# Optimization experiments

Measured on AMD Instinct MI355X. Metric: run time of the kernel, lower is better.

The kernel has to match this reference:

```python
import jax, jax.numpy as jnp
import numpy as np
import math

B, S, D = 4, 2048, 1024

def setup_inputs() -> dict:
    key = jax.random.key(0)
    k_x, k_q, k_k, k_v = jax.random.split(key, 4)
    scale = 1.0 / math.sqrt(D)
    return {
        "x": jax.random.normal(k_x, (B, S, D), dtype=jnp.float32),
        "W_Q": jax.random.normal(k_q, (D, D), dtype=jnp.float32) * scale,
        "W_K": jax.random.normal(k_k, (D, D), dtype=jnp.float32) * scale,
        "W_V": jax.random.normal(k_v, (D, D), dtype=jnp.float32) * scale,
    }

def reference(x, W_Q, W_K, W_V):
    # nn.Linear(bias=False): y = x @ W.T
    Q = jnp.einsum('bsd,ed->bse', x, W_Q)
    K = jnp.einsum('bsd,ed->bse', x, W_K)
    V = jnp.einsum('bsd,ed->bse', x, W_V)
    scores = jnp.einsum('bqd,bkd->bqk', Q, K) / jnp.sqrt(jnp.asarray(Q.shape[-1], Q.dtype))
    weight = jax.nn.softmax(scores, axis=-1)  # [B,S,S]
    return jnp.einsum('bqk,bkd->bqd', weight, V)
```

## Files before the change

### kernel.cpp

```cpp
#include <hip/hip_runtime.h>
#include <stdint.h>

typedef __bf16 bf16;
typedef __bf16 bf16x8 __attribute__((ext_vector_type(8)));
typedef __bf16 bf16x4 __attribute__((ext_vector_type(4)));
typedef float f32x4 __attribute__((ext_vector_type(4)));

__device__ inline void gload_lds16(const void* g, void* l) {
  __builtin_amdgcn_global_load_lds(
      (__attribute__((address_space(1))) void*)g,
      (__attribute__((address_space(3))) void*)l, 16, 0, 0);
}

__global__ __launch_bounds__(256) void cvt_all(
    const float* __restrict__ x, const float* __restrict__ wq,
    const float* __restrict__ wk, const float* __restrict__ wv,
    bf16* __restrict__ xb, bf16* __restrict__ Wb) {
  const int NX = 2097152;
  const int NW = 262144;
  int i = blockIdx.x * 256 + threadIdx.x;
  const int stride = gridDim.x * 256;
  for (int p = i; p < NX + 3 * NW; p += stride) {
    const float* src; bf16* dst; int off;
    if (p < NX) { src = x; dst = xb; off = p; }
    else {
      int q = p - NX; int w = q >> 18; off = q & (NW - 1);
      src = (w == 0) ? wq : ((w == 1) ? wk : wv);
      dst = Wb + (long)w * 1048576;
    }
    float4 v = ((const float4*)src)[off];
    bf16x4 o;
    o[0] = (bf16)v.x; o[1] = (bf16)v.y; o[2] = (bf16)v.z; o[3] = (bf16)v.w;
    ((bf16x4*)dst)[off] = o;
  }
}

__global__ __launch_bounds__(512, 2) void projT(
    const bf16* __restrict__ Wg, const bf16* __restrict__ Xg,
    bf16* __restrict__ QKbuf, bf16* __restrict__ Vt)
{
  constexpr int BUFSZ = 40960;
  __shared__ alignas(16) char lds[2 * BUFSZ];
  const int tid = threadIdx.x;
  const int l = tid & 63;
  const int wv = tid >> 6;
  const int wm = wv >> 2;
  const int wn = wv & 3;
  const int fr = l & 15;
  const int kch = l >> 4;
  const int m0 = blockIdx.y * 384;
  const int n0 = blockIdx.x * 256;

  const int a_rd = fr * 128 + (((wm * 4 + kch) ^ (fr & 7)) << 4);
  const int b_rd = 24576 + (wn & 1) * 8192 + fr * 128 + ((((wn >> 1) * 4 + kch) ^ (fr & 7)) << 4);

  const int se = (tid & 7) ^ ((tid >> 3) & 7);
  const int s_rowA = (se >> 2) * 192 + (tid >> 3);
  const int s_rowB = (se >> 2) * 128 + (tid >> 3);
  const int s_k = (se & 3) * 8;
  const int wb16 = (tid & 448) * 16;

  const int NT = 32;
  f32x4 acc[12][4] = {};

  auto stageA = [&](int tile, int buf, int rd) {
    gload_lds16(Wg + (long)(m0 + s_rowA + rd * 64) * 1024 + tile * 32 + s_k,
                lds + buf * BUFSZ + rd * 8192 + wb16);
  };
  auto stageB = [&](int tile, int buf, int rd) {
    gload_lds16(Xg + (long)(n0 + s_rowB + rd * 64) * 1024 + tile * 32 + s_k,
                lds + buf * BUFSZ + 24576 + rd * 8192 + wb16);
  };

  stageA(0, 0, 0); stageB(0, 0, 0); stageA(0, 0, 1); stageB(0, 0, 1); stageA(0, 0, 2);
  stageA(1, 1, 0); stageB(1, 1, 0); stageA(1, 1, 1);
  asm volatile("s_waitcnt vmcnt(3)" ::: "memory");
  __builtin_amdgcn_sched_barrier(0);
  __builtin_amdgcn_s_barrier();

  for (int t = 0; t < NT; ++t) {
    const char* buf = lds + (t & 1) * BUFSZ;
    const int t1 = min(t + 1, NT - 1);
    const int t2 = min(t + 2, NT - 1);
    const int nb = (t & 1) ^ 1;
    const int cur = t & 1;

    bf16x8 bfg[4], af[4];
    stageA(t1, nb, 2); stageB(t1, nb, 1);
#pragma unroll
    for (int n = 0; n < 4; ++n) bfg[n] = *(const bf16x8*)(buf + n * 2048 + b_rd);
#pragma unroll
    for (int m = 0; m < 4; ++m) af[m] = *(const bf16x8*)(buf + m * 2048 + a_rd);
    __builtin_amdgcn_s_barrier();
    __builtin_amdgcn_s_setprio(1);
#pragma unroll
    for (int m = 0; m < 4; ++m)
#pragma unroll
      for (int n = 0; n < 4; ++n)
        acc[m][n] = __builtin_amdgcn_mfma_f32_16x16x32_bf16(af[m], bfg[n], acc[m][n], 0, 0, 0);
    __builtin_amdgcn_s_setprio(0);
    __builtin_amdgcn_s_barrier();
    stageA(t2, cur, 0); stageB(t2, cur, 0);
#pragma unroll
    for (int m = 0; m < 4; ++m) af[m] = *(const bf16x8*)(buf + 8192 + m * 2048 + a_rd);
    __builtin_amdgcn_s_barrier();
    __builtin_amdgcn_s_setprio(1);
#pragma unroll
    for (int m = 0; m < 4; ++m)
#pragma unroll
      for (int n = 0; n < 4; ++n)
        acc[4 + m][n] = __builtin_amdgcn_mfma_f32_16x16x32_bf16(af[m], bfg[n], acc[4 + m][n], 0, 0, 0);
    __builtin_amdgcn_s_setprio(0);
    __builtin_amdgcn_s_barrier();
    stageA(t2, cur, 1);
#pragma unroll
    for (int m = 0; m < 4; ++m) af[m] = *(const bf16x8*)(buf + 16384 + m * 2048 + a_rd);
    __builtin_amdgcn_s_barrier();
    __builtin_amdgcn_s_setprio(1);
#pragma unroll
    for (int m = 0; m < 4; ++m)
#pragma unroll
      for (int n = 0; n < 4; ++n)
        acc[8 + m][n] = __builtin_amdgcn_mfma_f32_16x16x32_bf16(af[m], bfg[n], acc[8 + m][n], 0, 0, 0);
    __builtin_amdgcn_s_setprio(0);
    asm volatile("s_waitcnt vmcnt(3)" ::: "memory");
    __builtin_amdgcn_sched_barrier(0);
    __builtin_amdgcn_s_barrier();
  }
  asm volatile("s_waitcnt vmcnt(0)" ::: "memory");

#pragma unroll
  for (int mf = 0; mf < 12; ++mf) {
    const int wrow = m0 + wm * 192 + (mf >> 2) * 64 + (mf & 3) * 16 + (l >> 4) * 4;
#pragma unroll
    for (int n = 0; n < 4; ++n) {
      const int xrow = n0 + wn * 64 + n * 16 + fr;
      if (wrow < 2048) {
        bf16x4 pk;
#pragma unroll
        for (int r = 0; r < 4; ++r) pk[r] = (bf16)acc[mf][n][r];
        *(bf16x4*)(QKbuf + (long)xrow * 2048 + wrow) = pk;
      } else {
        const int b = xrow >> 11;
        const int s = xrow & 2047;
#pragma unroll
        for (int r = 0; r < 4; ++r)
          Vt[(long)b * 2097152 + (long)(wrow - 2048 + r) * 2048 + s] = (bf16)acc[mf][n][r];
      }
    }
  }
}

__global__ __launch_bounds__(512, 2) void gemm8(
    const bf16* __restrict__ Ag, const bf16* __restrict__ Bg,
    bf16* __restrict__ Cg,
    long lda, long ldb, long ldc,
    long sA, long sB, long sC, int K, float scale)
{
  constexpr int BUFSZ = 65536;
  __shared__ alignas(16) char lds[2 * BUFSZ];
  const int tid = threadIdx.x;
  const int l = tid & 63;
  const int wv = tid >> 6;
  const int fr = l & 15;
  const int kch = l >> 4;
  const int m0 = blockIdx.y * 256;
  const int n0 = blockIdx.x * 256;
  const bf16* Ab = Ag + (long)blockIdx.z * sA;
  const bf16* Bb = Bg + (long)blockIdx.z * sB;

  const int wm = wv >> 2;
  const int wn = wv & 3;

  const int a_rd = fr * 128 + (((wm * 4 + kch) ^ (fr & 7)) << 4);
  const int b_rd = (wn & 1) * 8192 + fr * 128 + ((((wn >> 1) * 4 + kch) ^ (fr & 7)) << 4);

  const int se = (tid & 7) ^ ((tid >> 3) & 7);
  const int s_row = (se >> 2) * 128 + (tid >> 3);
  const int s_k = (se & 3) * 8;
  const int wb16 = (tid & 448) * 16;

  const int NT = K >> 6;
  f32x4 acc[8][4] = {};

  auto stageA = [&](int tile, int kh, int buf) {
#pragma unroll
    for (int rd = 0; rd < 2; ++rd)
      gload_lds16(Ab + (long)(m0 + s_row + rd * 64) * lda + tile * 64 + kh * 32 + s_k,
                  lds + buf * BUFSZ + kh * 16384 + rd * 8192 + wb16);
  };
  auto stageB = [&](int tile, int kh, int buf) {
#pragma unroll
    for (int rd = 0; rd < 2; ++rd)
      gload_lds16(Bb + (long)(n0 + s_row + rd * 64) * ldb + tile * 64 + kh * 32 + s_k,
                  lds + buf * BUFSZ + 32768 + kh * 16384 + rd * 8192 + wb16);
  };

  stageA(0, 0, 0); stageB(0, 0, 0); stageA(0, 1, 0); stageB(0, 1, 0);
  stageA(min(1, NT - 1), 0, 1); stageB(min(1, NT - 1), 0, 1);
  asm volatile("s_waitcnt vmcnt(4)" ::: "memory");
  __builtin_amdgcn_sched_barrier(0);
  __builtin_amdgcn_s_barrier();

  for (int t = 0; t < NT; ++t) {
    const char* bufA = lds + (t & 1) * BUFSZ;
    const char* bufB = bufA + 32768;
    const int t1 = min(t + 1, NT - 1);
    const int t2 = min(t + 2, NT - 1);
    const int nb = (t & 1) ^ 1;
    const int cur = t & 1;

    bf16x8 bfg[4], af[4];
    stageA(t1, 1, nb);
#pragma unroll
    for (int n = 0; n < 4; ++n) bfg[n] = *(const bf16x8*)(bufB + n * 2048 + b_rd);
#pragma unroll
    for (int m = 0; m < 4; ++m) af[m] = *(const bf16x8*)(bufA + m * 2048 + a_rd);
    __builtin_amdgcn_s_barrier();
    __builtin_amdgcn_s_setprio(1);
#pragma unroll
    for (int m = 0; m < 4; ++m)
#pragma unroll
      for (int n = 0; n < 4; ++n)
        acc[m][n] = __builtin_amdgcn_mfma_f32_16x16x32_bf16(af[m], bfg[n], acc[m][n], 0, 0, 0);
    __builtin_amdgcn_s_setprio(0);
    __builtin_amdgcn_s_barrier();
    stageB(t1, 1, nb);
#pragma unroll
    for (int m = 0; m < 4; ++m) af[m] = *(const bf16x8*)(bufA + 8192 + m * 2048 + a_rd);
    __builtin_amdgcn_s_barrier();
    __builtin_amdgcn_s_setprio(1);
#pragma unroll
    for (int m = 0; m < 4; ++m)
#pragma unroll
      for (int n = 0; n < 4; ++n)
        acc[4 + m][n] = __builtin_amdgcn_mfma_f32_16x16x32_bf16(af[m], bfg[n], acc[4 + m][n], 0, 0, 0);
    __builtin_amdgcn_s_setprio(0);
    __builtin_amdgcn_s_barrier();
    stageA(t2, 0, cur);
#pragma unroll
    for (int n = 0; n < 4; ++n) bfg[n] = *(const bf16x8*)(bufB + 16384 + n * 2048 + b_rd);
#pragma unroll
    for (int m = 0; m < 4; ++m) af[m] = *(const bf16x8*)(bufA + 16384 + m * 2048 + a_rd);
    __builtin_amdgcn_s_barrier();
    __builtin_amdgcn_s_setprio(1);
#pragma unroll
    for (int m = 0; m < 4; ++m)
#pragma unroll
      for (int n = 0; n < 4; ++n)
        acc[m][n] = __builtin_amdgcn_mfma_f32_16x16x32_bf16(af[m], bfg[n], acc[m][n], 0, 0, 0);
    __builtin_amdgcn_s_setprio(0);
    __builtin_amdgcn_s_barrier();
    stageB(t2, 0, cur);
#pragma unroll
    for (int m = 0; m < 4; ++m) af[m] = *(const bf16x8*)(bufA + 16384 + 8192 + m * 2048 + a_rd);
    __builtin_amdgcn_s_barrier();
    __builtin_amdgcn_s_setprio(1);
#pragma unroll
    for (int m = 0; m < 4; ++m)
#pragma unroll
      for (int n = 0; n < 4; ++n)
        acc[4 + m][n] = __builtin_amdgcn_mfma_f32_16x16x32_bf16(af[m], bfg[n], acc[4 + m][n], 0, 0, 0);
    __builtin_amdgcn_s_setprio(0);
    asm volatile("s_waitcnt vmcnt(4)" ::: "memory");
    __builtin_amdgcn_sched_barrier(0);
    __builtin_amdgcn_s_barrier();
  }
  asm volatile("s_waitcnt vmcnt(0)" ::: "memory");

#pragma unroll
  for (int mf = 0; mf < 8; ++mf) {
    const int row = m0 + wm * 128 + (mf >> 2) * 64 + (mf & 3) * 16 + (l >> 4) * 4;
#pragma unroll
    for (int n = 0; n < 4; ++n) {
      const int col = n0 + wn * 64 + n * 16 + fr;
      bf16* C = Cg + (long)blockIdx.z * sC;
#pragma unroll
      for (int r = 0; r < 4; ++r)
        C[(long)(row + r) * ldc + col] = (bf16)(acc[mf][n][r] * scale);
    }
  }
}

__global__ __launch_bounds__(256, 2) void gemm2h(
    const bf16* __restrict__ Ag, const bf16* __restrict__ Bg,
    float* __restrict__ Cg,
    long lda, long ldb, long ldc,
    long sA, long sB, long sC, int K)
{
  constexpr int BUFSZ = 32768;
  __shared__ alignas(16) char lds[2 * BUFSZ];
  const int tid = threadIdx.x;
  const int l = tid & 63;
  const int wv = tid >> 6;
  const int wm = wv >> 1, wn = wv & 1;
  const int fr = l & 15;
  const int kch = l >> 4;
  const int m0 = blockIdx.y * 128;
  const int n0 = blockIdx.x * 128;
  const bf16* Ab = Ag + (long)blockIdx.z * sA;
  const bf16* Bb = Bg + (long)blockIdx.z * sB;

  const int a_rd = fr * 128 + (((wm * 4 + kch) ^ (fr & 7)) << 4);
  const int b_rd = fr * 128 + (((wn * 4 + kch) ^ (fr & 7)) << 4);

  const int se = (tid & 7) ^ ((tid >> 3) & 7);
  const int s_row = (se >> 2) * 64 + (tid >> 3);
  const int s_k = (se & 3) * 8;
  const int wb16 = (tid >> 6) * 1024;

  const int NT = K >> 6;
  f32x4 acc[4][4] = {};

  auto stageA = [&](int tile, int kh, int buf) {
#pragma unroll
    for (int rd = 0; rd < 2; ++rd)
      gload_lds16(Ab + (long)(m0 + s_row + rd * 32) * lda + tile * 64 + kh * 32 + s_k,
                  lds + buf * BUFSZ + kh * 8192 + rd * 4096 + wb16);
  };
  auto stageB = [&](int tile, int kh, int buf) {
#pragma unroll
    for (int rd = 0; rd < 2; ++rd)
      gload_lds16(Bb + (long)(n0 + s_row + rd * 32) * ldb + tile * 64 + kh * 32 + s_k,
                  lds + buf * BUFSZ + 16384 + kh * 8192 + rd * 4096 + wb16);
  };

  stageA(0, 0, 0); stageB(0, 0, 0); stageA(0, 1, 0); stageB(0, 1, 0);
  stageA(min(1, NT - 1), 0, 1); stageB(min(1, NT - 1), 0, 1);
  asm volatile("s_waitcnt vmcnt(4)" ::: "memory");
  __builtin_amdgcn_sched_barrier(0);
  __builtin_amdgcn_s_barrier();

  for (int t = 0; t < NT; ++t) {
    const char* bufA = lds + (t & 1) * BUFSZ;
    const char* bufB = bufA + 16384;
    const int t1 = min(t + 1, NT - 1);
    const int t2 = min(t + 2, NT - 1);
    const int nb = (t & 1) ^ 1;
    const int cur = t & 1;

    bf16x8 bfg[4], af[4];
    stageA(t1, 1, nb); stageB(t1, 1, nb);
#pragma unroll
    for (int n = 0; n < 4; ++n) bfg[n] = *(const bf16x8*)(bufB + n * 2048 + b_rd);
#pragma unroll
    for (int m = 0; m < 4; ++m) af[m] = *(const bf16x8*)(bufA + m * 2048 + a_rd);
    __builtin_amdgcn_s_barrier();
    __builtin_amdgcn_s_setprio(1);
#pragma unroll
    for (int m = 0; m < 4; ++m)
#pragma unroll
      for (int n = 0; n < 4; ++n)
        acc[m][n] = __builtin_amdgcn_mfma_f32_16x16x32_bf16(af[m], bfg[n], acc[m][n], 0, 0, 0);
    __builtin_amdgcn_s_setprio(0);
    __builtin_amdgcn_s_barrier();
    stageA(t2, 0, cur); stageB(t2, 0, cur);
#pragma unroll
    for (int n = 0; n < 4; ++n) bfg[n] = *(const bf16x8*)(bufB + 8192 + n * 2048 + b_rd);
#pragma unroll
    for (int m = 0; m < 4; ++m) af[m] = *(const bf16x8*)(bufA + 8192 + m * 2048 + a_rd);
    __builtin_amdgcn_s_barrier();
    __builtin_amdgcn_s_setprio(1);
#pragma unroll
    for (int m = 0; m < 4; ++m)
#pragma unroll
      for (int n = 0; n < 4; ++n)
        acc[m][n] = __builtin_amdgcn_mfma_f32_16x16x32_bf16(af[m], bfg[n], acc[m][n], 0, 0, 0);
    __builtin_amdgcn_s_setprio(0);
    asm volatile("s_waitcnt vmcnt(4)" ::: "memory");
    __builtin_amdgcn_sched_barrier(0);
    __builtin_amdgcn_s_barrier();
  }
  asm volatile("s_waitcnt vmcnt(0)" ::: "memory");

#pragma unroll
  for (int mf = 0; mf < 4; ++mf) {
    const int row = m0 + wm * 64 + mf * 16 + (l >> 4) * 4;
#pragma unroll
    for (int n = 0; n < 4; ++n) {
      const int col = n0 + wn * 64 + n * 16 + fr;
      float* C = Cg + (long)blockIdx.z * sC;
#pragma unroll
      for (int r = 0; r < 4; ++r)
        C[(long)(row + r) * ldc + col] = acc[mf][n][r];
    }
  }
}

__global__ __launch_bounds__(256) void softmax_k(const bf16* __restrict__ Sm,
                                                 bf16* __restrict__ P, int cols) {
  __shared__ float red[8];
  const long row = blockIdx.x;
  const bf16* sr = Sm + row * (long)cols;
  bf16* pr = P + row * (long)cols;
  const int t = threadIdx.x;
  bf16x8 v = *(const bf16x8*)(sr + t * 8);
  float e[8];
#pragma unroll
  for (int j = 0; j < 8; ++j) e[j] = (float)v[j];
  float m = e[0];
#pragma unroll
  for (int j = 1; j < 8; ++j) m = fmaxf(m, e[j]);
#pragma unroll
  for (int o = 32; o; o >>= 1) m = fmaxf(m, __shfl_xor(m, o));
  if ((t & 63) == 0) red[t >> 6] = m;
  __syncthreads();
  m = fmaxf(fmaxf(red[0], red[1]), fmaxf(red[2], red[3]));
  float s = 0.f;
#pragma unroll
  for (int j = 0; j < 8; ++j) { e[j] = __expf(e[j] - m); s += e[j]; }
#pragma unroll
  for (int o = 32; o; o >>= 1) s += __shfl_xor(s, o);
  if ((t & 63) == 0) red[4 + (t >> 6)] = s;
  __syncthreads();
  s = red[4] + red[5] + red[6] + red[7];
  const float inv = 1.0f / s;
  bf16x8 o8;
#pragma unroll
  for (int j = 0; j < 8; ++j) o8[j] = (bf16)(e[j] * inv);
  *(bf16x8*)(pr + t * 8) = o8;
}

extern "C" void kernel_launch(void* const* d_in, const int* in_sizes, int n_in,
                              void* d_out, int out_size, void* d_ws, size_t ws_size,
                              hipStream_t stream) {
  const float* x  = (const float*)d_in[0];
  const float* Wq = (const float*)d_in[1];
  const float* Wk = (const float*)d_in[2];
  const float* Wv = (const float*)d_in[3];
  float* out = (float*)d_out;

  char* ws = (char*)d_ws;
  bf16* QKbuf = (bf16*)(ws);
  bf16* P     = (bf16*)(ws);
  bf16* Vt    = (bf16*)(ws + 33554432);
  bf16* scb   = (bf16*)(ws + 50331648);
  bf16* xb    = (bf16*)(ws + 50331648);
  bf16* Wb    = (bf16*)(ws + 67108864);

  dim3 b256(256, 1, 1), b512(512, 1, 1);

  cvt_all<<<2048, b256, 0, stream>>>(x, Wq, Wk, Wv, xb, Wb);

  projT<<<dim3(32, 8, 1), b512, 0, stream>>>(Wb, xb, QKbuf, Vt);

  gemm8<<<dim3(8, 8, 4), b512, 0, stream>>>(
      QKbuf, QKbuf + 1024, scb, 2048, 2048, 2048,
      4194304, 4194304, 4194304, 1024, 0.03125f);

  softmax_k<<<8192, b256, 0, stream>>>(scb, P, 2048);

  gemm2h<<<dim3(8, 16, 4), b256, 0, stream>>>(
      P, Vt, out, 2048, 2048, 1024,
      4194304, 2097152, 2097152, 2048);
}
```

Baseline: 167.6 us.

## Swap projection GEMM operand roles and drop redundant LDS barriers in GEMMs

The projection kernel is rewritten so that x is the M-side operand and the stacked weights are the N-side operand. Each wave now computes an 8x6 fragment tile over two sub-steps per K tile instead of 12x4 over three, and the QK outputs are written row-major with scalar stores while V^T gets packed vector stores. Separately, the barrier between the LDS fragment reads and the MFMA block is removed in the projection, gemm8 and gemm2h loops, which cuts per-iteration synchronisation. Removing those barriers relies on the remaining barriers and vmcnt waits to keep the double-buffered LDS reads safe, and there is a risk of a race if buffer reuse ordering was depending on them.

```diff
diff --git a/kernel.cpp b/kernel.cpp
--- a/kernel.cpp
+++ b/kernel.cpp
@@ -35,8 +35,8 @@
   }
 }
 
-__global__ __launch_bounds__(512, 2) void projT(
-    const bf16* __restrict__ Wg, const bf16* __restrict__ Xg,
+__global__ __launch_bounds__(512, 2) void projW(
+    const bf16* __restrict__ Xg, const bf16* __restrict__ Wg,
     bf16* __restrict__ QKbuf, bf16* __restrict__ Vt)
 {
   constexpr int BUFSZ = 40960;
@@ -48,104 +48,100 @@
   const int wn = wv & 3;
   const int fr = l & 15;
   const int kch = l >> 4;
-  const int m0 = blockIdx.y * 384;
-  const int n0 = blockIdx.x * 256;
+  const int m0 = blockIdx.y * 256;
+  const int n0 = blockIdx.x * 384;
 
   const int a_rd = fr * 128 + (((wm * 4 + kch) ^ (fr & 7)) << 4);
-  const int b_rd = 24576 + (wn & 1) * 8192 + fr * 128 + ((((wn >> 1) * 4 + kch) ^ (fr & 7)) << 4);
+  int b_off[6];
+#pragma unroll
+  for (int n = 0; n < 6; ++n) {
+    const int rowbase = wn * 96 + n * 16;
+    const int half = rowbase >= 192 ? 1 : 0;
+    b_off[n] = 16384 + (rowbase - half * 192 + fr) * 128 +
+               (((half * 4 + kch) ^ (fr & 7)) << 4);
+  }
 
   const int se = (tid & 7) ^ ((tid >> 3) & 7);
-  const int s_rowA = (se >> 2) * 192 + (tid >> 3);
-  const int s_rowB = (se >> 2) * 128 + (tid >> 3);
+  const int s_rowA = (se >> 2) * 128 + (tid >> 3);
+  const int s_rowB = (se >> 2) * 192 + (tid >> 3);
   const int s_k = (se & 3) * 8;
   const int wb16 = (tid & 448) * 16;
 
-  const int NT = 32;
-  f32x4 acc[12][4] = {};
+  f32x4 acc[8][6] = {};
 
   auto stageA = [&](int tile, int buf, int rd) {
-    gload_lds16(Wg + (long)(m0 + s_rowA + rd * 64) * 1024 + tile * 32 + s_k,
+    gload_lds16(Xg + (long)(m0 + s_rowA + rd * 64) * 1024 + tile * 32 + s_k,
                 lds + buf * BUFSZ + rd * 8192 + wb16);
   };
   auto stageB = [&](int tile, int buf, int rd) {
-    gload_lds16(Xg + (long)(n0 + s_rowB + rd * 64) * 1024 + tile * 32 + s_k,
-                lds + buf * BUFSZ + 24576 + rd * 8192 + wb16);
-  };
-
-  stageA(0, 0, 0); stageB(0, 0, 0); stageA(0, 0, 1); stageB(0, 0, 1); stageA(0, 0, 2);
-  stageA(1, 1, 0); stageB(1, 1, 0); stageA(1, 1, 1);
-  asm volatile("s_waitcnt vmcnt(3)" ::: "memory");
+    gload_lds16(Wg + (long)(n0 + s_rowB + rd * 64) * 1024 + tile * 32 + s_k,
+                lds + buf * BUFSZ + 16384 + rd * 8192 + wb16);
+  };
+
+  stageA(0, 0, 0); stageA(0, 0, 1);
+  stageB(0, 0, 0); stageB(0, 0, 1); stageB(0, 0, 2);
+  stageA(1, 1, 0);
+  stageB(1, 1, 0); stageB(1, 1, 1); stageB(1, 1, 2);
+  asm volatile("s_waitcnt vmcnt(4)" ::: "memory");
   __builtin_amdgcn_sched_barrier(0);
   __builtin_amdgcn_s_barrier();
 
-  for (int t = 0; t < NT; ++t) {
+  for (int t = 0; t < 32; ++t) {
     const char* buf = lds + (t & 1) * BUFSZ;
-    const int t1 = min(t + 1, NT - 1);
-    const int t2 = min(t + 2, NT - 1);
+    const int t1 = min(t + 1, 31);
+    const int t2 = min(t + 2, 31);
     const int nb = (t & 1) ^ 1;
     const int cur = t & 1;
 
-    bf16x8 bfg[4], af[4];
-    stageA(t1, nb, 2); stageB(t1, nb, 1);
-#pragma unroll
-    for (int n = 0; n < 4; ++n) bfg[n] = *(const bf16x8*)(buf + n * 2048 + b_rd);
+    bf16x8 bfg[6], af[4];
+    stageA(t1, nb, 1);
+    asm volatile("s_waitcnt vmcnt(5)" ::: "memory");
+    __builtin_amdgcn_sched_barrier(0);
+#pragma unroll
+    for (int n = 0; n < 6; ++n) bfg[n] = *(const bf16x8*)(buf + b_off[n]);
 #pragma unroll
     for (int m = 0; m < 4; ++m) af[m] = *(const bf16x8*)(buf + m * 2048 + a_rd);
-    __builtin_amdgcn_s_barrier();
-    __builtin_amdgcn_s_setprio(1);
-#pragma unroll
-    for (int m = 0; m < 4; ++m)
-#pragma unroll
-      for (int n = 0; n < 4; ++n)
+    __builtin_amdgcn_s_setprio(1);
+#pragma unroll
+    for (int m = 0; m < 4; ++m)
+#pragma unroll
+      for (int n = 0; n < 6; ++n)
         acc[m][n] = __builtin_amdgcn_mfma_f32_16x16x32_bf16(af[m], bfg[n], acc[m][n], 0, 0, 0);
     __builtin_amdgcn_s_setprio(0);
     __builtin_amdgcn_s_barrier();
-    stageA(t2, cur, 0); stageB(t2, cur, 0);
-#pragma unroll
-    for (int m = 0; m < 4; ++m) af[m] = *(const bf16x8*)(buf + 8192 + m * 2048 + a_rd);
-    __builtin_amdgcn_s_barrier();
-    __builtin_amdgcn_s_setprio(1);
-#pragma unroll
-    for (int m = 0; m < 4; ++m)
-#pragma unroll
-      for (int n = 0; n < 4; ++n)
+    stageA(t2, cur, 0);
+    stageB(t2, cur, 0); stageB(t2, cur, 1); stageB(t2, cur, 2);
+#pragma unroll
+    for (int m = 0; m < 4; ++m) af[m] = *(const bf16x8*)(buf + (4 + m) * 2048 + a_rd);
+    __builtin_amdgcn_s_setprio(1);
+#pragma unroll
+    for (int m = 0; m < 4; ++m)
+#pragma unroll
+      for (int n = 0; n < 6; ++n)
         acc[4 + m][n] = __builtin_amdgcn_mfma_f32_16x16x32_bf16(af[m], bfg[n], acc[4 + m][n], 0, 0, 0);
     __builtin_amdgcn_s_setprio(0);
     __builtin_amdgcn_s_barrier();
-    stageA(t2, cur, 1);
-#pragma unroll
-    for (int m = 0; m < 4; ++m) af[m] = *(const bf16x8*)(buf + 16384 + m * 2048 + a_rd);
-    __builtin_amdgcn_s_barrier();
-    __builtin_amdgcn_s_setprio(1);
-#pragma unroll
-    for (int m = 0; m < 4; ++m)
-#pragma unroll
-      for (int n = 0; n < 4; ++n)
-        acc[8 + m][n] = __builtin_amdgcn_mfma_f32_16x16x32_bf16(af[m], bfg[n], acc[8 + m][n], 0, 0, 0);
-    __builtin_amdgcn_s_setprio(0);
-    asm volatile("s_waitcnt vmcnt(3)" ::: "memory");
-    __builtin_amdgcn_sched_barrier(0);
-    __builtin_amdgcn_s_barrier();
   }
   asm volatile("s_waitcnt vmcnt(0)" ::: "memory");
 
 #pragma unroll
-  for (int mf = 0; mf < 12; ++mf) {
-    const int wrow = m0 + wm * 192 + (mf >> 2) * 64 + (mf & 3) * 16 + (l >> 4) * 4;
-#pragma unroll
-    for (int n = 0; n < 4; ++n) {
-      const int xrow = n0 + wn * 64 + n * 16 + fr;
-      if (wrow < 2048) {
+  for (int mf = 0; mf < 8; ++mf) {
+    const int row = m0 + wm * 128 + mf * 16 + (l >> 4) * 4;
+#pragma unroll
+    for (int n = 0; n < 6; ++n) {
+      const int col = n0 + wn * 96 + n * 16 + fr;
+      if (col < 2048) {
+#pragma unroll
+        for (int r = 0; r < 4; ++r)
+          QKbuf[(long)(row + r) * 2048 + col] = (bf16)acc[mf][n][r];
+      } else {
+        const int b = row >> 11;
+        const int s = row & 2047;
+        const int d = col - 2048;
         bf16x4 pk;
 #pragma unroll
         for (int r = 0; r < 4; ++r) pk[r] = (bf16)acc[mf][n][r];
-        *(bf16x4*)(QKbuf + (long)xrow * 2048 + wrow) = pk;
-      } else {
-        const int b = xrow >> 11;
-        const int s = xrow & 2047;
-#pragma unroll
-        for (int r = 0; r < 4; ++r)
-          Vt[(long)b * 2097152 + (long)(wrow - 2048 + r) * 2048 + s] = (bf16)acc[mf][n][r];
+        *(bf16x4*)(Vt + (long)b * 2097152 + (long)d * 2048 + s) = pk;
       }
     }
   }
@@ -216,7 +212,6 @@
     for (int n = 0; n < 4; ++n) bfg[n] = *(const bf16x8*)(bufB + n * 2048 + b_rd);
 #pragma unroll
     for (int m = 0; m < 4; ++m) af[m] = *(const bf16x8*)(bufA + m * 2048 + a_rd);
-    __builtin_amdgcn_s_barrier();
     __builtin_amdgcn_s_setprio(1);
 #pragma unroll
     for (int m = 0; m < 4; ++m)
@@ -228,7 +223,6 @@
     stageB(t1, 1, nb);
 #pragma unroll
     for (int m = 0; m < 4; ++m) af[m] = *(const bf16x8*)(bufA + 8192 + m * 2048 + a_rd);
-    __builtin_amdgcn_s_barrier();
     __builtin_amdgcn_s_setprio(1);
 #pragma unroll
     for (int m = 0; m < 4; ++m)
@@ -242,7 +236,6 @@
     for (int n = 0; n < 4; ++n) bfg[n] = *(const bf16x8*)(bufB + 16384 + n * 2048 + b_rd);
 #pragma unroll
     for (int m = 0; m < 4; ++m) af[m] = *(const bf16x8*)(bufA + 16384 + m * 2048 + a_rd);
-    __builtin_amdgcn_s_barrier();
     __builtin_amdgcn_s_setprio(1);
 #pragma unroll
     for (int m = 0; m < 4; ++m)
@@ -254,7 +247,6 @@
     stageB(t2, 0, cur);
 #pragma unroll
     for (int m = 0; m < 4; ++m) af[m] = *(const bf16x8*)(bufA + 16384 + 8192 + m * 2048 + a_rd);
-    __builtin_amdgcn_s_barrier();
     __builtin_amdgcn_s_setprio(1);
 #pragma unroll
     for (int m = 0; m < 4; ++m)
@@ -345,7 +337,6 @@
     for (int n = 0; n < 4; ++n) bfg[n] = *(const bf16x8*)(bufB + n * 2048 + b_rd);
 #pragma unroll
     for (int m = 0; m < 4; ++m) af[m] = *(const bf16x8*)(bufA + m * 2048 + a_rd);
-    __builtin_amdgcn_s_barrier();
     __builtin_amdgcn_s_setprio(1);
 #pragma unroll
     for (int m = 0; m < 4; ++m)
@@ -359,7 +350,6 @@
     for (int n = 0; n < 4; ++n) bfg[n] = *(const bf16x8*)(bufB + 8192 + n * 2048 + b_rd);
 #pragma unroll
     for (int m = 0; m < 4; ++m) af[m] = *(const bf16x8*)(bufA + 8192 + m * 2048 + a_rd);
-    __builtin_amdgcn_s_barrier();
     __builtin_amdgcn_s_setprio(1);
 #pragma unroll
     for (int m = 0; m < 4; ++m)
@@ -442,7 +432,7 @@
 
   cvt_all<<<2048, b256, 0, stream>>>(x, Wq, Wk, Wv, xb, Wb);
 
-  projT<<<dim3(32, 8, 1), b512, 0, stream>>>(Wb, xb, QKbuf, Vt);
+  projW<<<dim3(8, 32, 1), b512, 0, stream>>>(xb, Wb, QKbuf, Vt);
 
   gemm8<<<dim3(8, 8, 4), b512, 0, stream>>>(
       QKbuf, QKbuf + 1024, scb, 2048, 2048, 2048,
```

New measurement: 168.8 us. No clear change (+0.7%).

## Split fused QKV projection into gemm8 for QK and dedicated projV kernel

Applied to the files above, without the earlier changes.

Replaces the single transposed projection kernel (384x256 tiles, with a scattered scalar Vt store) with two launches. The generic gemm8 computes Q and K as x@W^T into QKbuf, and a new projV kernel computes V with 256x128 tiles and a K-step of 64, writing Vt with packed 4-element stores. It also removes the barrier between the LDS fragment reads and the MFMA phases in gemm8 and gemm2h, cutting synchronisation. This adds one kernel launch, and dropping those barriers depends on the remaining barriers still ordering buffer reuse correctly.

```diff
diff --git a/kernel.cpp b/kernel.cpp
--- a/kernel.cpp
+++ b/kernel.cpp
@@ -35,122 +35,6 @@
   }
 }
 
-__global__ __launch_bounds__(512, 2) void projT(
-    const bf16* __restrict__ Wg, const bf16* __restrict__ Xg,
-    bf16* __restrict__ QKbuf, bf16* __restrict__ Vt)
-{
-  constexpr int BUFSZ = 40960;
-  __shared__ alignas(16) char lds[2 * BUFSZ];
-  const int tid = threadIdx.x;
-  const int l = tid & 63;
-  const int wv = tid >> 6;
-  const int wm = wv >> 2;
-  const int wn = wv & 3;
-  const int fr = l & 15;
-  const int kch = l >> 4;
-  const int m0 = blockIdx.y * 384;
-  const int n0 = blockIdx.x * 256;
-
-  const int a_rd = fr * 128 + (((wm * 4 + kch) ^ (fr & 7)) << 4);
-  const int b_rd = 24576 + (wn & 1) * 8192 + fr * 128 + ((((wn >> 1) * 4 + kch) ^ (fr & 7)) << 4);
-
-  const int se = (tid & 7) ^ ((tid >> 3) & 7);
-  const int s_rowA = (se >> 2) * 192 + (tid >> 3);
-  const int s_rowB = (se >> 2) * 128 + (tid >> 3);
-  const int s_k = (se & 3) * 8;
-  const int wb16 = (tid & 448) * 16;
-
-  const int NT = 32;
-  f32x4 acc[12][4] = {};
-
-  auto stageA = [&](int tile, int buf, int rd) {
-    gload_lds16(Wg + (long)(m0 + s_rowA + rd * 64) * 1024 + tile * 32 + s_k,
-                lds + buf * BUFSZ + rd * 8192 + wb16);
-  };
-  auto stageB = [&](int tile, int buf, int rd) {
-    gload_lds16(Xg + (long)(n0 + s_rowB + rd * 64) * 1024 + tile * 32 + s_k,
-                lds + buf * BUFSZ + 24576 + rd * 8192 + wb16);
-  };
-
-  stageA(0, 0, 0); stageB(0, 0, 0); stageA(0, 0, 1); stageB(0, 0, 1); stageA(0, 0, 2);
-  stageA(1, 1, 0); stageB(1, 1, 0); stageA(1, 1, 1);
-  asm volatile("s_waitcnt vmcnt(3)" ::: "memory");
-  __builtin_amdgcn_sched_barrier(0);
-  __builtin_amdgcn_s_barrier();
-
-  for (int t = 0; t < NT; ++t) {
-    const char* buf = lds + (t & 1) * BUFSZ;
-    const int t1 = min(t + 1, NT - 1);
-    const int t2 = min(t + 2, NT - 1);
-    const int nb = (t & 1) ^ 1;
-    const int cur = t & 1;
-
-    bf16x8 bfg[4], af[4];
-    stageA(t1, nb, 2); stageB(t1, nb, 1);
-#pragma unroll
-    for (int n = 0; n < 4; ++n) bfg[n] = *(const bf16x8*)(buf + n * 2048 + b_rd);
-#pragma unroll
-    for (int m = 0; m < 4; ++m) af[m] = *(const bf16x8*)(buf + m * 2048 + a_rd);
-    __builtin_amdgcn_s_barrier();
-    __builtin_amdgcn_s_setprio(1);
-#pragma unroll
-    for (int m = 0; m < 4; ++m)
-#pragma unroll
-      for (int n = 0; n < 4; ++n)
-        acc[m][n] = __builtin_amdgcn_mfma_f32_16x16x32_bf16(af[m], bfg[n], acc[m][n], 0, 0, 0);
-    __builtin_amdgcn_s_setprio(0);
-    __builtin_amdgcn_s_barrier();
-    stageA(t2, cur, 0); stageB(t2, cur, 0);
-#pragma unroll
-    for (int m = 0; m < 4; ++m) af[m] = *(const bf16x8*)(buf + 8192 + m * 2048 + a_rd);
-    __builtin_amdgcn_s_barrier();
-    __builtin_amdgcn_s_setprio(1);
-#pragma unroll
-    for (int m = 0; m < 4; ++m)
-#pragma unroll
-      for (int n = 0; n < 4; ++n)
-        acc[4 + m][n] = __builtin_amdgcn_mfma_f32_16x16x32_bf16(af[m], bfg[n], acc[4 + m][n], 0, 0, 0);
-    __builtin_amdgcn_s_setprio(0);
-    __builtin_amdgcn_s_barrier();
-    stageA(t2, cur, 1);
-#pragma unroll
-    for (int m = 0; m < 4; ++m) af[m] = *(const bf16x8*)(buf + 16384 + m * 2048 + a_rd);
-    __builtin_amdgcn_s_barrier();
-    __builtin_amdgcn_s_setprio(1);
-#pragma unroll
-    for (int m = 0; m < 4; ++m)
-#pragma unroll
-      for (int n = 0; n < 4; ++n)
-        acc[8 + m][n] = __builtin_amdgcn_mfma_f32_16x16x32_bf16(af[m], bfg[n], acc[8 + m][n], 0, 0, 0);
-    __builtin_amdgcn_s_setprio(0);
-    asm volatile("s_waitcnt vmcnt(3)" ::: "memory");
-    __builtin_amdgcn_sched_barrier(0);
-    __builtin_amdgcn_s_barrier();
-  }
-  asm volatile("s_waitcnt vmcnt(0)" ::: "memory");
-
-#pragma unroll
-  for (int mf = 0; mf < 12; ++mf) {
-    const int wrow = m0 + wm * 192 + (mf >> 2) * 64 + (mf & 3) * 16 + (l >> 4) * 4;
-#pragma unroll
-    for (int n = 0; n < 4; ++n) {
-      const int xrow = n0 + wn * 64 + n * 16 + fr;
-      if (wrow < 2048) {
-        bf16x4 pk;
-#pragma unroll
-        for (int r = 0; r < 4; ++r) pk[r] = (bf16)acc[mf][n][r];
-        *(bf16x4*)(QKbuf + (long)xrow * 2048 + wrow) = pk;
-      } else {
-        const int b = xrow >> 11;
-        const int s = xrow & 2047;
-#pragma unroll
-        for (int r = 0; r < 4; ++r)
-          Vt[(long)b * 2097152 + (long)(wrow - 2048 + r) * 2048 + s] = (bf16)acc[mf][n][r];
-      }
-    }
-  }
-}
-
 __global__ __launch_bounds__(512, 2) void gemm8(
     const bf16* __restrict__ Ag, const bf16* __restrict__ Bg,
     bf16* __restrict__ Cg,
@@ -216,7 +100,6 @@
     for (int n = 0; n < 4; ++n) bfg[n] = *(const bf16x8*)(bufB + n * 2048 + b_rd);
 #pragma unroll
     for (int m = 0; m < 4; ++m) af[m] = *(const bf16x8*)(bufA + m * 2048 + a_rd);
-    __builtin_amdgcn_s_barrier();
     __builtin_amdgcn_s_setprio(1);
 #pragma unroll
     for (int m = 0; m < 4; ++m)
@@ -228,7 +111,6 @@
     stageB(t1, 1, nb);
 #pragma unroll
     for (int m = 0; m < 4; ++m) af[m] = *(const bf16x8*)(bufA + 8192 + m * 2048 + a_rd);
-    __builtin_amdgcn_s_barrier();
     __builtin_amdgcn_s_setprio(1);
 #pragma unroll
     for (int m = 0; m < 4; ++m)
@@ -242,7 +124,6 @@
     for (int n = 0; n < 4; ++n) bfg[n] = *(const bf16x8*)(bufB + 16384 + n * 2048 + b_rd);
 #pragma unroll
     for (int m = 0; m < 4; ++m) af[m] = *(const bf16x8*)(bufA + 16384 + m * 2048 + a_rd);
-    __builtin_amdgcn_s_barrier();
     __builtin_amdgcn_s_setprio(1);
 #pragma unroll
     for (int m = 0; m < 4; ++m)
@@ -254,7 +135,6 @@
     stageB(t2, 0, cur);
 #pragma unroll
     for (int m = 0; m < 4; ++m) af[m] = *(const bf16x8*)(bufA + 16384 + 8192 + m * 2048 + a_rd);
-    __builtin_amdgcn_s_barrier();
     __builtin_amdgcn_s_setprio(1);
 #pragma unroll
     for (int m = 0; m < 4; ++m)
@@ -278,6 +158,132 @@
 #pragma unroll
       for (int r = 0; r < 4; ++r)
         C[(long)(row + r) * ldc + col] = (bf16)(acc[mf][n][r] * scale);
+    }
+  }
+}
+
+__global__ __launch_bounds__(512, 2) void projV(
+    const bf16* __restrict__ Xg, const bf16* __restrict__ Wv,
+    bf16* __restrict__ Vt)
+{
+  constexpr int BUFSZ = 49152;
+  __shared__ alignas(16) char lds[2 * BUFSZ];
+  const int tid = threadIdx.x;
+  const int l = tid & 63;
+  const int wv = tid >> 6;
+  const int wm = wv >> 2;
+  const int wn = wv & 3;
+  const int fr = l & 15;
+  const int kch = l >> 4;
+  const int m0 = blockIdx.y * 256;
+  const int n0 = blockIdx.x * 128;
+
+  const int a_rd = fr * 128 + (((wm * 4 + kch) ^ (fr & 7)) << 4);
+  int b_off[2];
+#pragma unroll
+  for (int n = 0; n < 2; ++n)
+    b_off[n] = 32768 + ((wn & 1) * 32 + n * 16 + fr) * 128 +
+               ((((wn >> 1) * 4 + kch) ^ (fr & 7)) << 4);
+
+  const int se = (tid & 7) ^ ((tid >> 3) & 7);
+  const int s_rowA = (se >> 2) * 128 + (tid >> 3);
+  const int s_rowB = (se >> 2) * 64 + (tid >> 3);
+  const int s_k = (se & 3) * 8;
+  const int wb16 = (tid & 448) * 16;
+
+  const int NT = 16;
+  f32x4 acc[8][2] = {};
+
+  auto stageA = [&](int tile, int kh, int buf) {
+#pragma unroll
+    for (int rd = 0; rd < 2; ++rd)
+      gload_lds16(Xg + (long)(m0 + s_rowA + rd * 64) * 1024 + tile * 64 + kh * 32 + s_k,
+                  lds + buf * BUFSZ + kh * 16384 + rd * 8192 + wb16);
+  };
+  auto stageB = [&](int tile, int kh, int buf) {
+    gload_lds16(Wv + (long)(n0 + s_rowB) * 1024 + tile * 64 + kh * 32 + s_k,
+                lds + buf * BUFSZ + 32768 + kh * 8192 + wb16);
+  };
+
+  stageA(0, 0, 0); stageB(0, 0, 0); stageA(0, 1, 0); stageB(0, 1, 0);
+  stageA(1, 0, 1); stageB(1, 0, 1);
+  asm volatile("s_waitcnt vmcnt(3)" ::: "memory");
+  __builtin_amdgcn_sched_barrier(0);
+  __builtin_amdgcn_s_barrier();
+
+  for (int t = 0; t < NT; ++t) {
+    const char* bufA = lds + (t & 1) * BUFSZ;
+    const int t1 = min(t + 1, NT - 1);
+    const int t2 = min(t + 2, NT - 1);
+    const int nb = (t & 1) ^ 1;
+    const int cur = t & 1;
+
+    bf16x8 bfg[2], af[4];
+    stageA(t1, 1, nb);
+#pragma unroll
+    for (int n = 0; n < 2; ++n) bfg[n] = *(const bf16x8*)(bufA + b_off[n]);
+#pragma unroll
+    for (int m = 0; m < 4; ++m) af[m] = *(const bf16x8*)(bufA + m * 2048 + a_rd);
+    __builtin_amdgcn_s_setprio(1);
+#pragma unroll
+    for (int m = 0; m < 4; ++m)
+#pragma unroll
+      for (int n = 0; n < 2; ++n)
+        acc[m][n] = __builtin_amdgcn_mfma_f32_16x16x32_bf16(af[m], bfg[n], acc[m][n], 0, 0, 0);
+    __builtin_amdgcn_s_setprio(0);
+    __builtin_amdgcn_s_barrier();
+    stageB(t1, 1, nb);
+#pragma unroll
+    for (int m = 0; m < 4; ++m) af[m] = *(const bf16x8*)(bufA + 8192 + m * 2048 + a_rd);
+    __builtin_amdgcn_s_setprio(1);
+#pragma unroll
+    for (int m = 0; m < 4; ++m)
+#pragma unroll
+      for (int n = 0; n < 2; ++n)
+        acc[4 + m][n] = __builtin_amdgcn_mfma_f32_16x16x32_bf16(af[m], bfg[n], acc[4 + m][n], 0, 0, 0);
+    __builtin_amdgcn_s_setprio(0);
+    __builtin_amdgcn_s_barrier();
+    stageA(t2, 0, cur);
+#pragma unroll
+    for (int n = 0; n < 2; ++n) bfg[n] = *(const bf16x8*)(bufA + 8192 + b_off[n]);
+#pragma unroll
+    for (int m = 0; m < 4; ++m) af[m] = *(const bf16x8*)(bufA + 16384 + m * 2048 + a_rd);
+    __builtin_amdgcn_s_setprio(1);
+#pragma unroll
+    for (int m = 0; m < 4; ++m)
+#pragma unroll
+      for (int n = 0; n < 2; ++n)
+        acc[m][n] = __builtin_amdgcn_mfma_f32_16x16x32_bf16(af[m], bfg[n], acc[m][n], 0, 0, 0);
+    __builtin_amdgcn_s_setprio(0);
+    __builtin_amdgcn_s_barrier();
+    stageB(t2, 0, cur);
+#pragma unroll
+    for (int m = 0; m < 4; ++m) af[m] = *(const bf16x8*)(bufA + 16384 + 8192 + m * 2048 + a_rd);
+    __builtin_amdgcn_s_setprio(1);
+#pragma unroll
+    for (int m = 0; m < 4; ++m)
+#pragma unroll
+      for (int n = 0; n < 2; ++n)
+        acc[4 + m][n] = __builtin_amdgcn_mfma_f32_16x16x32_bf16(af[m], bfg[n], acc[4 + m][n], 0, 0, 0);
+    __builtin_amdgcn_s_setprio(0);
+    asm volatile("s_waitcnt vmcnt(3)" ::: "memory");
+    __builtin_amdgcn_sched_barrier(0);
+    __builtin_amdgcn_s_barrier();
+  }
+  asm volatile("s_waitcnt vmcnt(0)" ::: "memory");
+
+#pragma unroll
+  for (int mf = 0; mf < 8; ++mf) {
+    const int row = m0 + wm * 128 + (mf >> 2) * 64 + (mf & 3) * 16 + (l >> 4) * 4;
+    const int b = row >> 11;
+    const int s = row & 2047;
+#pragma unroll
+    for (int n = 0; n < 2; ++n) {
+      const int d = n0 + wn * 32 + n * 16 + fr;
+      bf16x4 pk;
+#pragma unroll
+      for (int r = 0; r < 4; ++r) pk[r] = (bf16)acc[mf][n][r];
+      *(bf16x4*)(Vt + (long)b * 2097152 + (long)d * 2048 + s) = pk;
     }
   }
 }
@@ -345,7 +351,6 @@
     for (int n = 0; n < 4; ++n) bfg[n] = *(const bf16x8*)(bufB + n * 2048 + b_rd);
 #pragma unroll
     for (int m = 0; m < 4; ++m) af[m] = *(const bf16x8*)(bufA + m * 2048 + a_rd);
-    __builtin_amdgcn_s_barrier();
     __builtin_amdgcn_s_setprio(1);
 #pragma unroll
     for (int m = 0; m < 4; ++m)
@@ -359,7 +364,6 @@
     for (int n = 0; n < 4; ++n) bfg[n] = *(const bf16x8*)(bufB + 8192 + n * 2048 + b_rd);
 #pragma unroll
     for (int m = 0; m < 4; ++m) af[m] = *(const bf16x8*)(bufA + 8192 + m * 2048 + a_rd);
-    __builtin_amdgcn_s_barrier();
     __builtin_amdgcn_s_setprio(1);
 #pragma unroll
     for (int m = 0; m < 4; ++m)
@@ -442,7 +446,10 @@
 
   cvt_all<<<2048, b256, 0, stream>>>(x, Wq, Wk, Wv, xb, Wb);
 
-  projT<<<dim3(32, 8, 1), b512, 0, stream>>>(Wb, xb, QKbuf, Vt);
+  gemm8<<<dim3(8, 32, 1), b512, 0, stream>>>(
+      xb, Wb, QKbuf, 1024, 1024, 2048, 0, 0, 0, 1024, 1.f);
+
+  projV<<<dim3(8, 32, 1), b512, 0, stream>>>(xb, Wb + 2097152, Vt);
 
   gemm8<<<dim3(8, 8, 4), b512, 0, stream>>>(
       QKbuf, QKbuf + 1024, scb, 2048, 2048, 2048,
```

New measurement: 181.5 us. 1.08x slower.
